# Performance work log

Hardware: AMD Instinct MI355X
Metric: run time of the kernel (lower is better)

The kernel has to match this reference:

```python
import jax, jax.numpy as jnp
import numpy as np

ITERATIONS = 3
OUT_CAPS, OUT_DIM = 10, 16


def squash(x):
    # square_norm / (1 + square_norm) * x / (sqrt(square_norm) + 1e-6), norm over last axis
    sn = jnp.sum(x * x, axis=-1, keepdims=True)
    return sn / (1.0 + sn) * x / (jnp.sqrt(sn) + 1e-6)


def setup_inputs() -> dict:
    key = jax.random.key(0)
    kx, kw = jax.random.split(key)
    x = jax.random.normal(kx, (256, 32, 6, 6, 8), dtype=jnp.float32)
    W = 0.01 * jax.random.normal(kw, (1, 32, 6, 6, 10, 8, 16), dtype=jnp.float32)
    return {"x": x, "W": W}


def reference(x, W):
    w = W[0]  # [i,j,k,o,d,e]
    # u_hat: prediction vectors, [B, i, j, k, O, E]
    u_hat = jnp.einsum('bijkd,ijkode->bijkoe', x, w)
    u_det = jax.lax.stop_gradient(u_hat)
    b = jnp.zeros(u_hat.shape[:-1], dtype=u_hat.dtype)  # [B,i,j,k,O]
    for _ in range(ITERATIONS - 1):
        c = jax.nn.softmax(b, axis=-1)
        s = jnp.einsum('bijko,bijkoe->boe', c, u_det)   # reduce over all input-capsule axes
        v = squash(s)                                    # [B,O,E]
        b = b + jnp.einsum('bijkoe,boe->bijko', u_det, v)
    c = jax.nn.softmax(b, axis=-1)
    s = jnp.einsum('bijko,bijkoe->boe', c, u_hat)
    v = squash(s)
    return v.reshape(-1, OUT_CAPS, OUT_DIM)
```

## Files before the change

### kernel.cpp

```cpp
#include <hip/hip_runtime.h>
#include <math.h>

#define BATCH 256
#define IC    1152
#define DD    8
#define OO    10
#define EE    16
#define BTILE 64
#define NBT   4
#define NT    256
#define CHUNK 8
#define NCHUNK 144

typedef __attribute__((ext_vector_type(8))) short short8;
typedef __attribute__((ext_vector_type(4))) float f32x4;

__device__ __forceinline__ unsigned short f2bf(float f) {
    unsigned u = __float_as_uint(f);
    unsigned r = u + 0x7FFFu + ((u >> 16) & 1u);
    return (unsigned short)(r >> 16);
}
__device__ __forceinline__ float bf2f(unsigned short h) {
    return __uint_as_float(((unsigned)h) << 16);
}

__global__ __launch_bounds__(NT) void caps_pass_kernel(
    const float* __restrict__ x,
    const float* __restrict__ W,
    const float* __restrict__ V,
    float* __restrict__ s_part,
    int first)
{
    __shared__ __align__(16) char smem[57360];
    unsigned short* w_hi = (unsigned short*)(smem);
    unsigned short* w_lo = (unsigned short*)(smem + 20480);
    unsigned short* x_hi = (unsigned short*)(smem + 40960);
    unsigned short* x_lo = (unsigned short*)(smem + 49152);
    unsigned short* zpad = (unsigned short*)(smem + 57344);

    const int tid  = threadIdx.x;
    const int wv   = tid >> 6;
    const int lane = tid & 63;
    const int q    = lane >> 4;
    const int em   = lane & 15;
    const int ijk0 = blockIdx.x * CHUNK;
    const int bg0  = blockIdx.y * BTILE;

    if (tid < 4) ((unsigned*)zpad)[tid] = 0u;

    {
        const float4* wg4 = reinterpret_cast<const float4*>(W + (size_t)ijk0 * (OO*DD*EE));
        #pragma unroll
        for (int i = 0; i < 10; ++i) {
            const int f = tid + i * NT;
            const float4 t = wg4[f];
            const int l4 = f << 2;
            const int e0 = l4 & 15;
            int rr = l4 >> 4;
            const int d = rr & 7; rr >>= 3;
            const int o = rr % 10, s = rr / 10;
            const float vv[4] = {t.x, t.y, t.z, t.w};
            #pragma unroll
            for (int j = 0; j < 4; ++j) {
                const unsigned short h = f2bf(vv[j]);
                const unsigned short l = f2bf(vv[j] - bf2f(h));
                const int off = (s*160 + o*16 + e0 + j) * 8 + d;
                w_hi[off] = h; w_lo[off] = l;
            }
        }
    }
    {
        #pragma unroll
        for (int i = 0; i < 2; ++i) {
            const int u = tid + i * NT;
            const int b = u >> 3, s = u & 7;
            const float* xp = x + ((size_t)(bg0 + b) * IC + (ijk0 + s)) * DD;
            const float4 xa = *reinterpret_cast<const float4*>(xp);
            const float4 xb = *reinterpret_cast<const float4*>(xp + 4);
            const float vv[8] = {xa.x,xa.y,xa.z,xa.w, xb.x,xb.y,xb.z,xb.w};
            short8 hv, lv;
            #pragma unroll
            for (int j = 0; j < 8; ++j) {
                const unsigned short h = f2bf(vv[j]);
                hv[j] = (short)h;
                lv[j] = (short)f2bf(vv[j] - bf2f(h));
            }
            const int off = (s*64 + b) * 8;
            *reinterpret_cast<short8*>(&x_hi[off]) = hv;
            *reinterpret_cast<short8*>(&x_lo[off]) = lv;
        }
    }

    f32x4 vreg[OO];
    if (!first) {
        const int bgl = bg0 + 16*wv + em;
        #pragma unroll
        for (int o = 0; o < OO; ++o) {
            const float4 t = *reinterpret_cast<const float4*>(
                V + (size_t)bgl * (OO*EE) + o*EE + 4*q);
            vreg[o] = (f32x4){t.x, t.y, t.z, t.w};
        }
    }

    __syncthreads();

    const unsigned short* wbase = (q==1) ? w_lo : ((q==3) ? zpad : w_hi);
    const unsigned short* xbase = (q==2) ? x_lo : ((q==3) ? zpad : x_hi);
    const int msk = (q==3) ? 0 : 1;

    f32x4 sacc[OO];
    #pragma unroll
    for (int o = 0; o < OO; ++o) sacc[o] = (f32x4){0.f,0.f,0.f,0.f};

    #pragma unroll 1
    for (int s = 0; s < CHUNK; ++s) {
        const short8 xf = *reinterpret_cast<const short8*>(
            xbase + msk * ((s*64 + 16*wv + em) * 8));
        f32x4 u[OO];
        #pragma unroll
        for (int o = 0; o < OO; ++o) {
            const short8 wf = *reinterpret_cast<const short8*>(
                wbase + msk * ((s*160 + o*16 + em) * 8));
            u[o] = __builtin_amdgcn_mfma_f32_16x16x32_bf16(
                       wf, xf, (f32x4){0.f,0.f,0.f,0.f}, 0, 0, 0);
        }
        if (!first) {
            float elg[OO];
            float den = 0.f;
            #pragma unroll
            for (int o = 0; o < OO; ++o) {
                float t = u[o][0]*vreg[o][0] + u[o][1]*vreg[o][1]
                        + u[o][2]*vreg[o][2] + u[o][3]*vreg[o][3];
                t += __shfl_xor(t, 16);
                t += __shfl_xor(t, 32);
                elg[o] = __expf(t);
                den += elg[o];
            }
            const float rden = __fdividef(1.0f, den);
            #pragma unroll
            for (int o = 0; o < OO; ++o)
                sacc[o] += u[o] * (elg[o] * rden);
        } else {
            #pragma unroll
            for (int o = 0; o < OO; ++o) sacc[o] += u[o];
        }
    }

    __syncthreads();
    float* sout = (float*)smem;
    const float mul = first ? 0.1f : 1.0f;
    {
        const int bl = 16*wv + em;
        #pragma unroll
        for (int o = 0; o < OO; ++o)
            #pragma unroll
            for (int r = 0; r < 4; ++r)
                sout[bl*168 + o*16 + 4*q + r] = mul * sacc[o][r];
    }
    __syncthreads();
    {
        float* sp = s_part + ((size_t)blockIdx.x * BATCH + bg0) * (OO*EE);
        #pragma unroll
        for (int i = 0; i < 10; ++i) {
            const int f = tid + i*NT;
            const int b = f / 40, c4 = (f % 40) * 4;
            const float4 t = *reinterpret_cast<const float4*>(&sout[b*168 + c4]);
            *reinterpret_cast<float4*>(&sp[(size_t)b*(OO*EE) + c4]) = t;
        }
    }
}

__global__ __launch_bounds__(256) void caps_squash_kernel(
    const float* __restrict__ s_part,
    float* __restrict__ V,
    float* __restrict__ out,
    int accum, int last)
{
    __shared__ float red[3][64];
    const int lane = threadIdx.x & 63;
    const int w    = threadIdx.x >> 6;
    const int g    = blockIdx.x * 64 + lane;

    const float* sp = s_part + g;
    float s = 0.f;
    #pragma unroll 4
    for (int ch = w * (NCHUNK / 4); ch < (w + 1) * (NCHUNK / 4); ++ch)
        s += sp[(size_t)ch * (BATCH * OO * EE)];

    if (w > 0) red[w - 1][lane] = s;
    __syncthreads();
    if (w == 0) {
        s += red[0][lane] + red[1][lane] + red[2][lane];

        float sq = s * s;
        #pragma unroll
        for (int m = 1; m < 16; m <<= 1) sq += __shfl_xor(sq, m, 16);

        float scale = sq / (1.f + sq) / (sqrtf(sq) + 1e-6f);
        float v = scale * s;

        if (last)       out[g] = v;
        else if (accum) V[g]  += v;
        else            V[g]   = v;
    }
}

extern "C" void kernel_launch(void* const* d_in, const int* in_sizes, int n_in,
                              void* d_out, int out_size, void* d_ws, size_t ws_size,
                              hipStream_t stream) {
    const float* x = (const float*)d_in[0];
    const float* W = (const float*)d_in[1];
    float* out = (float*)d_out;

    float* s_part = (float*)d_ws;
    float* V      = s_part + (size_t)NCHUNK * BATCH * OO * EE;

    dim3 grid(NCHUNK, NBT), blk(NT);
    const int sq_blocks = (BATCH * OO * EE) / 64;

    caps_pass_kernel<<<grid, blk, 0, stream>>>(x, W, V, s_part, 1);
    caps_squash_kernel<<<sq_blocks, 256, 0, stream>>>(s_part, V, out, 0, 0);
    caps_pass_kernel<<<grid, blk, 0, stream>>>(x, W, V, s_part, 0);
    caps_squash_kernel<<<sq_blocks, 256, 0, stream>>>(s_part, V, out, 1, 0);
    caps_pass_kernel<<<grid, blk, 0, stream>>>(x, W, V, s_part, 0);
    caps_squash_kernel<<<sq_blocks, 256, 0, stream>>>(s_part, V, out, 0, 1);
}
```

Baseline: 150.7 us.

## Pre-split W to bf16 hi/lo once and stream fragments from global memory

Adds a prep kernel that converts W into bf16 hi/lo halves laid out as MFMA fragments, run once per call instead of once per routing pass and block. The pass kernel then reads W fragments straight from global memory with no LDS staging. It recomputes the MFMA in the softmax branch rather than keeping ten u tiles in registers, which lowers register pressure and allows occupancy 4. It also writes partial sums directly without an LDS transpose and widens the squash reduction to 1024 threads. In exchange it adds a kernel launch, uses more workspace, and doubles MFMA work in the non-first passes.

```diff
diff --git a/kernel.cpp b/kernel.cpp
--- a/kernel.cpp
+++ b/kernel.cpp
@@ -11,6 +11,8 @@
 #define NT    256
 #define CHUNK 8
 #define NCHUNK 144
+#define WPC   1280
+#define WHALF ((size_t)IC * WPC)
 
 typedef __attribute__((ext_vector_type(8))) short short8;
 typedef __attribute__((ext_vector_type(4))) float f32x4;
@@ -24,19 +26,42 @@
     return __uint_as_float(((unsigned)h) << 16);
 }
 
-__global__ __launch_bounds__(NT) void caps_pass_kernel(
+__global__ __launch_bounds__(256) void caps_prep_kernel(
+    const float* __restrict__ W,
+    unsigned short* __restrict__ w_hi,
+    unsigned short* __restrict__ w_lo,
+    unsigned short* __restrict__ wz)
+{
+    const int idx = blockIdx.x * 256 + threadIdx.x;
+    if (blockIdx.x == 0 && threadIdx.x < 8) wz[threadIdx.x] = 0;
+    const int ijk = idx / 160;
+    const int oe  = idx - ijk * 160;
+    const int o = oe >> 4, e = oe & 15;
+    const float* src = W + (size_t)ijk * WPC + o * 128 + e;
+    short8 hv, lv;
+    #pragma unroll
+    for (int d = 0; d < 8; ++d) {
+        const float f = src[d * 16];
+        const unsigned short h = f2bf(f);
+        hv[d] = (short)h;
+        lv[d] = (short)f2bf(f - bf2f(h));
+    }
+    *reinterpret_cast<short8*>(w_hi + (size_t)idx * 8) = hv;
+    *reinterpret_cast<short8*>(w_lo + (size_t)idx * 8) = lv;
+}
+
+__global__ __launch_bounds__(NT, 4) void caps_pass_kernel(
     const float* __restrict__ x,
-    const float* __restrict__ W,
+    const unsigned short* __restrict__ w_hi,
+    const unsigned short* __restrict__ w_lo,
+    const unsigned short* __restrict__ wz,
     const float* __restrict__ V,
     float* __restrict__ s_part,
     int first)
 {
-    __shared__ __align__(16) char smem[57360];
-    unsigned short* w_hi = (unsigned short*)(smem);
-    unsigned short* w_lo = (unsigned short*)(smem + 20480);
-    unsigned short* x_hi = (unsigned short*)(smem + 40960);
-    unsigned short* x_lo = (unsigned short*)(smem + 49152);
-    unsigned short* zpad = (unsigned short*)(smem + 57344);
+    __shared__ unsigned short x_hi[CHUNK][BTILE][8];
+    __shared__ unsigned short x_lo[CHUNK][BTILE][8];
+    __shared__ unsigned short zpad[8];
 
     const int tid  = threadIdx.x;
     const int wv   = tid >> 6;
@@ -46,91 +71,70 @@
     const int ijk0 = blockIdx.x * CHUNK;
     const int bg0  = blockIdx.y * BTILE;
 
-    if (tid < 4) ((unsigned*)zpad)[tid] = 0u;
-
-    {
-        const float4* wg4 = reinterpret_cast<const float4*>(W + (size_t)ijk0 * (OO*DD*EE));
-        #pragma unroll
-        for (int i = 0; i < 10; ++i) {
-            const int f = tid + i * NT;
-            const float4 t = wg4[f];
-            const int l4 = f << 2;
-            const int e0 = l4 & 15;
-            int rr = l4 >> 4;
-            const int d = rr & 7; rr >>= 3;
-            const int o = rr % 10, s = rr / 10;
-            const float vv[4] = {t.x, t.y, t.z, t.w};
-            #pragma unroll
-            for (int j = 0; j < 4; ++j) {
-                const unsigned short h = f2bf(vv[j]);
-                const unsigned short l = f2bf(vv[j] - bf2f(h));
-                const int off = (s*160 + o*16 + e0 + j) * 8 + d;
-                w_hi[off] = h; w_lo[off] = l;
-            }
-        }
-    }
-    {
-        #pragma unroll
-        for (int i = 0; i < 2; ++i) {
-            const int u = tid + i * NT;
-            const int b = u >> 3, s = u & 7;
-            const float* xp = x + ((size_t)(bg0 + b) * IC + (ijk0 + s)) * DD;
-            const float4 xa = *reinterpret_cast<const float4*>(xp);
-            const float4 xb = *reinterpret_cast<const float4*>(xp + 4);
-            const float vv[8] = {xa.x,xa.y,xa.z,xa.w, xb.x,xb.y,xb.z,xb.w};
-            short8 hv, lv;
-            #pragma unroll
-            for (int j = 0; j < 8; ++j) {
-                const unsigned short h = f2bf(vv[j]);
-                hv[j] = (short)h;
-                lv[j] = (short)f2bf(vv[j] - bf2f(h));
-            }
-            const int off = (s*64 + b) * 8;
-            *reinterpret_cast<short8*>(&x_hi[off]) = hv;
-            *reinterpret_cast<short8*>(&x_lo[off]) = lv;
-        }
+    if (tid < 8) zpad[tid] = 0;
+
+    #pragma unroll
+    for (int i = 0; i < 2; ++i) {
+        const int u = tid + i * NT;
+        const int b = u >> 3, s = u & 7;
+        const float* xp = x + ((size_t)(bg0 + b) * IC + (ijk0 + s)) * DD;
+        const float4 xa = *reinterpret_cast<const float4*>(xp);
+        const float4 xb = *reinterpret_cast<const float4*>(xp + 4);
+        const float vv[8] = {xa.x,xa.y,xa.z,xa.w, xb.x,xb.y,xb.z,xb.w};
+        short8 hv, lv;
+        #pragma unroll
+        for (int j = 0; j < 8; ++j) {
+            const unsigned short h = f2bf(vv[j]);
+            hv[j] = (short)h;
+            lv[j] = (short)f2bf(vv[j] - bf2f(h));
+        }
+        *reinterpret_cast<short8*>(&x_hi[s][b][0]) = hv;
+        *reinterpret_cast<short8*>(&x_lo[s][b][0]) = lv;
     }
 
     f32x4 vreg[OO];
+    const int b = bg0 + 16 * wv + em;
     if (!first) {
-        const int bgl = bg0 + 16*wv + em;
         #pragma unroll
         for (int o = 0; o < OO; ++o) {
             const float4 t = *reinterpret_cast<const float4*>(
-                V + (size_t)bgl * (OO*EE) + o*EE + 4*q);
+                V + (size_t)b * (OO * EE) + o * EE + 4 * q);
             vreg[o] = (f32x4){t.x, t.y, t.z, t.w};
         }
     }
-
     __syncthreads();
 
-    const unsigned short* wbase = (q==1) ? w_lo : ((q==3) ? zpad : w_hi);
-    const unsigned short* xbase = (q==2) ? x_lo : ((q==3) ? zpad : x_hi);
-    const int msk = (q==3) ? 0 : 1;
+    const unsigned short* wbase = (q == 1) ? w_lo : ((q == 3) ? wz : w_hi);
+    const unsigned short* xbase = (q == 2) ? &x_lo[0][0][0]
+                                : ((q == 3) ? zpad : &x_hi[0][0][0]);
+    const size_t wmsk = (q == 3) ? 0 : 1;
+    const int    xmsk = (q == 3) ? 0 : 1;
+
+    uintptr_t wb2i = (uintptr_t)wbase;
+    asm volatile("" : "+v"(wb2i));
+    const unsigned short* wbase2 = (const unsigned short*)wb2i;
 
     f32x4 sacc[OO];
     #pragma unroll
-    for (int o = 0; o < OO; ++o) sacc[o] = (f32x4){0.f,0.f,0.f,0.f};
+    for (int o = 0; o < OO; ++o) sacc[o] = (f32x4){0.f, 0.f, 0.f, 0.f};
 
     #pragma unroll 1
     for (int s = 0; s < CHUNK; ++s) {
         const short8 xf = *reinterpret_cast<const short8*>(
-            xbase + msk * ((s*64 + 16*wv + em) * 8));
-        f32x4 u[OO];
-        #pragma unroll
-        for (int o = 0; o < OO; ++o) {
-            const short8 wf = *reinterpret_cast<const short8*>(
-                wbase + msk * ((s*160 + o*16 + em) * 8));
-            u[o] = __builtin_amdgcn_mfma_f32_16x16x32_bf16(
-                       wf, xf, (f32x4){0.f,0.f,0.f,0.f}, 0, 0, 0);
-        }
+            xbase + xmsk * ((s * BTILE + 16 * wv + em) * 8));
+        const size_t woff = (size_t)(ijk0 + s) * WPC + (size_t)em * 8;
+
         if (!first) {
             float elg[OO];
             float den = 0.f;
             #pragma unroll
             for (int o = 0; o < OO; ++o) {
-                float t = u[o][0]*vreg[o][0] + u[o][1]*vreg[o][1]
-                        + u[o][2]*vreg[o][2] + u[o][3]*vreg[o][3];
+                const short8 wf = *reinterpret_cast<const short8*>(
+                    wbase + wmsk * (woff + o * 128));
+                const f32x4 u = __builtin_amdgcn_mfma_f32_16x16x32_bf16(
+                                    wf, xf, (f32x4){0.f,0.f,0.f,0.f}, 0, 0, 0);
+                float t = u[0]*vreg[o][0] + u[1]*vreg[o][1]
+                        + u[2]*vreg[o][2] + u[3]*vreg[o][3];
                 t += __shfl_xor(t, 16);
                 t += __shfl_xor(t, 32);
                 elg[o] = __expf(t);
@@ -138,66 +142,68 @@
             }
             const float rden = __fdividef(1.0f, den);
             #pragma unroll
-            for (int o = 0; o < OO; ++o)
-                sacc[o] += u[o] * (elg[o] * rden);
+            for (int o = 0; o < OO; ++o) {
+                const short8 wf = *reinterpret_cast<const short8*>(
+                    wbase2 + wmsk * (woff + o * 128));
+                const f32x4 u = __builtin_amdgcn_mfma_f32_16x16x32_bf16(
+                                    wf, xf, (f32x4){0.f,0.f,0.f,0.f}, 0, 0, 0);
+                sacc[o] += u * (elg[o] * rden);
+            }
         } else {
             #pragma unroll
-            for (int o = 0; o < OO; ++o) sacc[o] += u[o];
-        }
-    }
-
-    __syncthreads();
-    float* sout = (float*)smem;
-    const float mul = first ? 0.1f : 1.0f;
+            for (int o = 0; o < OO; ++o) {
+                const short8 wf = *reinterpret_cast<const short8*>(
+                    wbase + wmsk * (woff + o * 128));
+                const f32x4 u = __builtin_amdgcn_mfma_f32_16x16x32_bf16(
+                                    wf, xf, (f32x4){0.f,0.f,0.f,0.f}, 0, 0, 0);
+                sacc[o] += u;
+            }
+        }
+    }
+
     {
-        const int bl = 16*wv + em;
-        #pragma unroll
-        for (int o = 0; o < OO; ++o)
-            #pragma unroll
-            for (int r = 0; r < 4; ++r)
-                sout[bl*168 + o*16 + 4*q + r] = mul * sacc[o][r];
-    }
-    __syncthreads();
-    {
-        float* sp = s_part + ((size_t)blockIdx.x * BATCH + bg0) * (OO*EE);
-        #pragma unroll
-        for (int i = 0; i < 10; ++i) {
-            const int f = tid + i*NT;
-            const int b = f / 40, c4 = (f % 40) * 4;
-            const float4 t = *reinterpret_cast<const float4*>(&sout[b*168 + c4]);
-            *reinterpret_cast<float4*>(&sp[(size_t)b*(OO*EE) + c4]) = t;
-        }
-    }
-}
-
-__global__ __launch_bounds__(256) void caps_squash_kernel(
+        const float mul = first ? 0.1f : 1.0f;
+        float* sp = s_part + (((size_t)blockIdx.x * BATCH + b) * OO) * EE + 4 * q;
+        #pragma unroll
+        for (int o = 0; o < OO; ++o) {
+            const f32x4 t = sacc[o];
+            float4 w4;
+            w4.x = mul * t[0]; w4.y = mul * t[1];
+            w4.z = mul * t[2]; w4.w = mul * t[3];
+            *reinterpret_cast<float4*>(sp + o * EE) = w4;
+        }
+    }
+}
+
+__global__ __launch_bounds__(1024) void caps_squash_kernel(
     const float* __restrict__ s_part,
     float* __restrict__ V,
     float* __restrict__ out,
     int accum, int last)
 {
-    __shared__ float red[3][64];
+    __shared__ float red[15][64];
     const int lane = threadIdx.x & 63;
     const int w    = threadIdx.x >> 6;
     const int g    = blockIdx.x * 64 + lane;
 
     const float* sp = s_part + g;
     float s = 0.f;
-    #pragma unroll 4
-    for (int ch = w * (NCHUNK / 4); ch < (w + 1) * (NCHUNK / 4); ++ch)
-        s += sp[(size_t)ch * (BATCH * OO * EE)];
+    #pragma unroll
+    for (int i = 0; i < NCHUNK / 16; ++i)
+        s += sp[(size_t)(w * (NCHUNK / 16) + i) * (BATCH * OO * EE)];
 
     if (w > 0) red[w - 1][lane] = s;
     __syncthreads();
     if (w == 0) {
-        s += red[0][lane] + red[1][lane] + red[2][lane];
+        #pragma unroll
+        for (int i = 0; i < 15; ++i) s += red[i][lane];
 
         float sq = s * s;
         #pragma unroll
         for (int m = 1; m < 16; m <<= 1) sq += __shfl_xor(sq, m, 16);
 
-        float scale = sq / (1.f + sq) / (sqrtf(sq) + 1e-6f);
-        float v = scale * s;
+        const float scale = sq / (1.f + sq) / (sqrtf(sq) + 1e-6f);
+        const float v = scale * s;
 
         if (last)       out[g] = v;
         else if (accum) V[g]  += v;
@@ -214,14 +220,19 @@
 
     float* s_part = (float*)d_ws;
     float* V      = s_part + (size_t)NCHUNK * BATCH * OO * EE;
+    unsigned short* w_hi = (unsigned short*)(V + BATCH * OO * EE);
+    unsigned short* w_lo = w_hi + WHALF;
+    unsigned short* wz   = w_lo + WHALF;
 
     dim3 grid(NCHUNK, NBT), blk(NT);
     const int sq_blocks = (BATCH * OO * EE) / 64;
 
-    caps_pass_kernel<<<grid, blk, 0, stream>>>(x, W, V, s_part, 1);
-    caps_squash_kernel<<<sq_blocks, 256, 0, stream>>>(s_part, V, out, 0, 0);
-    caps_pass_kernel<<<grid, blk, 0, stream>>>(x, W, V, s_part, 0);
-    caps_squash_kernel<<<sq_blocks, 256, 0, stream>>>(s_part, V, out, 1, 0);
-    caps_pass_kernel<<<grid, blk, 0, stream>>>(x, W, V, s_part, 0);
-    caps_squash_kernel<<<sq_blocks, 256, 0, stream>>>(s_part, V, out, 0, 1);
-}
+    caps_prep_kernel<<<(IC * 160) / 256, 256, 0, stream>>>(W, w_hi, w_lo, wz);
+
+    caps_pass_kernel<<<grid, blk, 0, stream>>>(x, w_hi, w_lo, wz, V, s_part, 1);
+    caps_squash_kernel<<<sq_blocks, 1024, 0, stream>>>(s_part, V, out, 0, 0);
+    caps_pass_kernel<<<grid, blk, 0, stream>>>(x, w_hi, w_lo, wz, V, s_part, 0);
+    caps_squash_kernel<<<sq_blocks, 1024, 0, stream>>>(s_part, V, out, 1, 0);
+    caps_pass_kernel<<<grid, blk, 0, stream>>>(x, w_hi, w_lo, wz, V, s_part, 0);
+    caps_squash_kernel<<<sq_blocks, 1024, 0, stream>>>(s_part, V, out, 0, 1);
+}
```

Result: slower. 219.2 us (+45.4%).
